# Performance work log

Hardware: AMD Instinct MI355X
Metric: run time of the kernel (lower is better)

The kernel has to match this reference:

```python
import jax, jax.numpy as jnp
import numpy as np

B, CIN, H, W = 4, 1024, 64, 64
PLANES = 256
K = 3
DIL = 2
PAD = DIL * (K - 1) // 2  # = 2
EPS = 1e-5


def setup_inputs() -> dict:
    key = jax.random.key(0)
    ks = jax.random.split(key, 16)
    d = {}
    d['x'] = jax.random.normal(ks[0], (B, CIN, H, W), dtype=jnp.float32)
    # conv1: 1x1, inplanes->planes, no bias
    d['w1'] = jax.random.normal(ks[1], (PLANES, CIN), dtype=jnp.float32) * 0.02
    d['gamma1'] = jnp.ones((PLANES,), jnp.float32)
    d['beta1'] = jnp.zeros((PLANES,), jnp.float32)
    d['mean1'] = jax.random.normal(ks[2], (PLANES,), dtype=jnp.float32) * 0.1
    d['var1'] = jax.random.uniform(ks[3], (PLANES,), minval=0.5, maxval=1.5, dtype=jnp.float32)
    # deform_offset: 3x3 conv planes->18, with bias
    d['woff'] = jax.random.normal(ks[4], (18, PLANES, K, K), dtype=jnp.float32) * 0.01
    d['boff'] = jnp.zeros((18,), jnp.float32)
    # conv2 (deformable): 3x3 planes->planes, with bias
    d['w2'] = jax.random.normal(ks[5], (PLANES, PLANES, K, K), dtype=jnp.float32) * 0.02
    d['bconv2'] = jnp.zeros((PLANES,), jnp.float32)
    d['gamma2'] = jnp.ones((PLANES,), jnp.float32)
    d['beta2'] = jnp.zeros((PLANES,), jnp.float32)
    d['mean2'] = jax.random.normal(ks[6], (PLANES,), dtype=jnp.float32) * 0.1
    d['var2'] = jax.random.uniform(ks[7], (PLANES,), minval=0.5, maxval=1.5, dtype=jnp.float32)
    # conv3: 1x1 planes->planes*4, no bias
    d['w3'] = jax.random.normal(ks[8], (PLANES * 4, PLANES), dtype=jnp.float32) * 0.02
    d['gamma3'] = jnp.ones((PLANES * 4,), jnp.float32)
    d['beta3'] = jnp.zeros((PLANES * 4,), jnp.float32)
    d['mean3'] = jax.random.normal(ks[9], (PLANES * 4,), dtype=jnp.float32) * 0.1
    d['var3'] = jax.random.uniform(ks[10], (PLANES * 4,), minval=0.5, maxval=1.5, dtype=jnp.float32)
    return d


def _bn(x, gamma, beta, mean, var):
    # inference-mode BatchNorm over channel dim (NCHW)
    inv = jax.lax.rsqrt(var + EPS)
    return (x - mean[:, None, None]) * (inv * gamma)[:, None, None] + beta[:, None, None]


def _deform_conv(x, offset, w, b):
    # x: [B,C,H,W]; offset: [B,18,H,W] ordered (dy,dx) per kernel tap; w: [O,C,3,3]
    Bn, C, Hh, Ww = x.shape
    off = offset.reshape(Bn, K * K, 2, Hh, Ww)
    off_y, off_x = off[:, :, 0], off[:, :, 1]          # [B,9,H,W]
    kk = jnp.arange(K * K)
    base_y = (kk // K) * DIL - PAD                      # [9]
    base_x = (kk % K) * DIL - PAD
    ys = jnp.arange(Hh, dtype=x.dtype)
    xs = jnp.arange(Ww, dtype=x.dtype)
    py = base_y.astype(x.dtype)[None, :, None, None] + ys[None, None, :, None] + off_y
    px = base_x.astype(x.dtype)[None, :, None, None] + xs[None, None, None, :] + off_x

    def sample_one(img, py1, px1):
        # img [C,H,W]; py1/px1 [9,H,W] -> [C,9,H,W] bilinear with zero padding
        y0 = jnp.floor(py1)
        x0 = jnp.floor(px1)
        wy = py1 - y0
        wx = px1 - x0

        def gather(yc, xc):
            yi = yc.astype(jnp.int32)
            xi = xc.astype(jnp.int32)
            valid = ((yi >= 0) & (yi < Hh) & (xi >= 0) & (xi < Ww)).astype(img.dtype)
            yi = jnp.clip(yi, 0, Hh - 1)
            xi = jnp.clip(xi, 0, Ww - 1)
            return img[:, yi, xi] * valid[None]

        v00 = gather(y0, x0)
        v01 = gather(y0, x0 + 1)
        v10 = gather(y0 + 1, x0)
        v11 = gather(y0 + 1, x0 + 1)
        return (v00 * ((1 - wy) * (1 - wx))[None] + v01 * ((1 - wy) * wx)[None]
                + v10 * (wy * (1 - wx))[None] + v11 * (wy * wx)[None])

    sampled = jax.vmap(sample_one)(x, py, px)           # [B,C,9,H,W]
    out = jnp.einsum('bckhw,ock->bohw', sampled, w.reshape(w.shape[0], C, K * K))
    return out + b[None, :, None, None]


def reference(x, w1, gamma1, beta1, mean1, var1, woff, boff, w2, bconv2,
              gamma2, beta2, mean2, var2, w3, gamma3, beta3, mean3, var3):
    residual = x
    out = jnp.einsum('bchw,oc->bohw', x, w1)            # conv1 1x1
    out = jax.nn.relu(_bn(out, gamma1, beta1, mean1, var1))
    offset = jax.lax.conv_general_dilated(
        out, woff, window_strides=(1, 1), padding=((PAD, PAD), (PAD, PAD)),
        rhs_dilation=(DIL, DIL), dimension_numbers=('NCHW', 'OIHW', 'NCHW'))
    offset = offset + boff[None, :, None, None]
    out = _deform_conv(out, offset, w2, bconv2)
    out = jax.nn.relu(_bn(out, gamma2, beta2, mean2, var2))
    out = jnp.einsum('bchw,oc->bohw', out, w3)          # conv3 1x1
    out = _bn(out, gamma3, beta3, mean3, var3)
    return jax.nn.relu(out + residual)
```

## Files before the change

### kernel.cpp

```cpp
#include <hip/hip_runtime.h>

#define EPS_BN 1e-5f

typedef __bf16 bf16x8 __attribute__((ext_vector_type(8)));
typedef float f32x4 __attribute__((ext_vector_type(4)));

__device__ __forceinline__ unsigned short f2bf(float f) {
  union { float f; unsigned u; } v; v.f = f;
  unsigned r = v.u + 0x7fffu + ((v.u >> 16) & 1u);
  return (unsigned short)(r >> 16);
}
__device__ __forceinline__ float bf2f(unsigned short h) {
  union { unsigned u; float f; } v; v.u = ((unsigned)h) << 16;
  return v.f;
}

__global__ __launch_bounds__(256) void prep_all(
    const float* __restrict__ w1, const float* __restrict__ w2, const float* __restrict__ woff,
    const float* __restrict__ w3,
    const float* g1, const float* b1, const float* m1, const float* v1,
    const float* g2, const float* b2, const float* m2, const float* v2, const float* bconv2,
    const float* g3, const float* b3, const float* m3, const float* v3,
    unsigned short* __restrict__ w1b, unsigned short* __restrict__ w2r,
    uint4* __restrict__ act1Pz, unsigned short* __restrict__ wob,
    unsigned short* __restrict__ w3b, float* __restrict__ shift3,
    float* s1, float* h1, float* s2, float* h2) {
  int bid = blockIdx.x, tid = threadIdx.x;
  if (bid < 1024) {
    int i = bid * 256 + tid;
    w1b[i] = f2bf(w1[i]);
  } else if (bid < 3328) {
    int i = (bid - 1024) * 256 + tid;
    int o = i / 2304, r = i % 2304;
    int kk = r / 256, c = r % 256;
    w2r[i] = f2bf(w2[(size_t)o * 2304 + c * 9 + kk]);
  } else if (bid < 5640) {
    int i = (bid - 3328) * 256 + tid;
    if (i < 591872) act1Pz[i] = uint4{0, 0, 0, 0};
  } else if (bid < 5928) {
    int i = (bid - 5640) * 256 + tid;
    int o = i / 2304, r = i % 2304;
    int kk = r / 256, c = r % 256;
    wob[i] = (o < 18) ? f2bf(woff[(size_t)o * 2304 + c * 9 + kk]) : (unsigned short)0;
  } else if (bid < 6952) {
    int i = (bid - 5928) * 256 + tid;
    int o = i >> 8;
    float sc = rsqrtf(v3[o] + EPS_BN) * g3[o];
    w3b[i] = f2bf(w3[i] * sc);
  } else if (bid < 6956) {
    int c = (bid - 6952) * 256 + tid;
    float sc = rsqrtf(v3[c] + EPS_BN) * g3[c];
    shift3[c] = b3[c] - m3[c] * sc;
  } else {
    int c = tid;
    float sc1 = rsqrtf(v1[c] + EPS_BN) * g1[c];
    s1[c] = sc1; h1[c] = b1[c] - m1[c] * sc1;
    float sc2 = rsqrtf(v2[c] + EPS_BN) * g2[c];
    s2[c] = sc2; h2[c] = b2[c] + (bconv2[c] - m2[c]) * sc2;
  }
}

__global__ __launch_bounds__(256) void transpose_x(const float* __restrict__ x,
                                                   unsigned short* __restrict__ xT) {
  __shared__ float t[32][33];
  int b = blockIdx.z;
  int p0 = blockIdx.x * 32, c0 = blockIdx.y * 32;
  int tx = threadIdx.x & 31, ty = threadIdx.x >> 5;
  const float* xb = x + (size_t)b * 1024 * 4096;
#pragma unroll
  for (int j = 0; j < 4; ++j) {
    int c = c0 + ty + j * 8;
    t[ty + j * 8][tx] = xb[(size_t)c * 4096 + p0 + tx];
  }
  __syncthreads();
  unsigned short* xTb = xT + (size_t)b * 4096 * 1024;
  int pl = threadIdx.x >> 3;
  int cl = (threadIdx.x & 7) * 4;
  float v0 = t[cl][pl], v1 = t[cl + 1][pl], v2 = t[cl + 2][pl], v3 = t[cl + 3][pl];
  uint2 pk;
  pk.x = (unsigned)f2bf(v0) | ((unsigned)f2bf(v1) << 16);
  pk.y = (unsigned)f2bf(v2) | ((unsigned)f2bf(v3) << 16);
  *(uint2*)(xTb + (size_t)(p0 + pl) * 1024 + c0 + cl) = pk;
}

__global__ __launch_bounds__(256) void gemm_split(
    const unsigned short* __restrict__ A, const unsigned short* __restrict__ Bm,
    unsigned short* __restrict__ part, int M, int N, int K, int KH) {
  __shared__ __align__(16) char smem[32768];
  unsigned short* sA0 = (unsigned short*)smem;
  unsigned short* sB0 = (unsigned short*)(smem + 8192);
  unsigned short* sA1 = (unsigned short*)(smem + 16384);
  unsigned short* sB1 = (unsigned short*)(smem + 24576);
  float* tbuf = (float*)smem;
  int tid = threadIdx.x, lane = tid & 63, wv = tid >> 6;
  int z = blockIdx.z;
  int m0 = blockIdx.y * 128, n0 = blockIdx.x * 128;
  f32x4 acc[4][4] = {};
  int rowA = tid >> 2;
  int kcol = (tid & 3) * 8;
  int wm = wv & 1, wn = wv >> 1;
  int lane15 = lane & 15, quad8 = (lane >> 4) * 8, quad = lane >> 4;

#define GS_STAGE(dA, dB, K0)                                                              \
  {                                                                                       \
    int k0_ = (K0);                                                                       \
    _Pragma("unroll") for (int r = 0; r < 2; ++r) {                                       \
      const unsigned short* gp = A + (size_t)(m0 + r * 64 + rowA) * K + k0_ + kcol;       \
      __builtin_amdgcn_global_load_lds((const __attribute__((address_space(1))) void*)gp, \
          (__attribute__((address_space(3))) void*)&(dA)[r * 2048 + wv * 512], 16, 0, 0); \
    }                                                                                     \
    _Pragma("unroll") for (int r = 0; r < 2; ++r) {                                       \
      const unsigned short* gp = Bm + (size_t)(n0 + r * 64 + rowA) * K + k0_ + kcol;      \
      __builtin_amdgcn_global_load_lds((const __attribute__((address_space(1))) void*)gp, \
          (__attribute__((address_space(3))) void*)&(dB)[r * 2048 + wv * 512], 16, 0, 0); \
    }                                                                                     \
  }

#define GS_COMPUTE(dA, dB)                                                                \
  {                                                                                       \
    bf16x8 afr[4], bfr[4];                                                                \
    _Pragma("unroll") for (int mi = 0; mi < 4; ++mi)                                      \
      afr[mi] = *(const bf16x8*)&(dA)[(wm * 64 + mi * 16 + lane15) * 32 + quad8];         \
    _Pragma("unroll") for (int ni = 0; ni < 4; ++ni)                                      \
      bfr[ni] = *(const bf16x8*)&(dB)[(wn * 64 + ni * 16 + lane15) * 32 + quad8];         \
    _Pragma("unroll") for (int mi = 0; mi < 4; ++mi)                                      \
      _Pragma("unroll") for (int ni = 0; ni < 4; ++ni)                                    \
        acc[mi][ni] =                                                                     \
            __builtin_amdgcn_mfma_f32_16x16x32_bf16(afr[mi], bfr[ni], acc[mi][ni], 0, 0, 0); \
  }

  int kbase = z * KH;
  int nst = KH >> 5;
  GS_STAGE(sA0, sB0, kbase);
  __syncthreads();
  for (int t = 0; t < nst; t += 2) {
    GS_STAGE(sA1, sB1, kbase + (t + 1) * 32);
    GS_COMPUTE(sA0, sB0);
    __syncthreads();
    if (t + 2 < nst) GS_STAGE(sA0, sB0, kbase + (t + 2) * 32);
    GS_COMPUTE(sA1, sB1);
    __syncthreads();
  }
#undef GS_STAGE
#undef GS_COMPUTE

  unsigned short* outH = part + (size_t)z * M * N;
  int trow = tid >> 3;
  int tcol16 = (tid & 7) * 16;
  int growBase = m0 + (trow >> 4) * 64 + (trow & 15);
#pragma unroll
  for (int mi = 0; mi < 4; ++mi) {
    __syncthreads();
#pragma unroll
    for (int ni = 0; ni < 4; ++ni)
#pragma unroll
      for (int reg = 0; reg < 4; ++reg)
        tbuf[(wm * 16 + quad * 4 + reg) * 132 + wn * 64 + ni * 16 + lane15] = acc[mi][ni][reg];
    __syncthreads();
    int gr = growBase + mi * 16;
    const float* lp = &tbuf[trow * 132 + tcol16];
    unsigned o[8];
#pragma unroll
    for (int j = 0; j < 8; ++j)
      o[j] = (unsigned)f2bf(lp[2 * j]) | ((unsigned)f2bf(lp[2 * j + 1]) << 16);
    unsigned short* op = outH + (size_t)gr * 256 + n0 + tcol16;
    *(uint4*)(op) = uint4{o[0], o[1], o[2], o[3]};
    *(uint4*)(op + 8) = uint4{o[4], o[5], o[6], o[7]};
  }
}

template <int NS, int PAD>
__global__ __launch_bounds__(256) void epi_bn(const unsigned short* __restrict__ part,
                                              const float* __restrict__ scale,
                                              const float* __restrict__ shift,
                                              unsigned short* __restrict__ outT,
                                              unsigned short* __restrict__ outP) {
  int gid = blockIdx.x * 256 + threadIdx.x;
  int row = gid >> 5, c0 = (gid & 31) * 8;
  float v[8] = {};
#pragma unroll
  for (int s = 0; s < NS; ++s) {
    uint4 q = *(const uint4*)(part + (size_t)s * 16384 * 256 + (size_t)row * 256 + c0);
    unsigned u[4] = {q.x, q.y, q.z, q.w};
#pragma unroll
    for (int j = 0; j < 4; ++j) {
      v[2 * j]     += bf2f((unsigned short)(u[j] & 0xffffu));
      v[2 * j + 1] += bf2f((unsigned short)(u[j] >> 16));
    }
  }
  float sc[8], sh[8];
  *(float4*)&sc[0] = *(const float4*)(scale + c0); *(float4*)&sc[4] = *(const float4*)(scale + c0 + 4);
  *(float4*)&sh[0] = *(const float4*)(shift + c0); *(float4*)&sh[4] = *(const float4*)(shift + c0 + 4);
  unsigned o[4];
#pragma unroll
  for (int j = 0; j < 4; ++j) {
    float lo = fmaxf(v[2 * j] * sc[2 * j] + sh[2 * j], 0.f);
    float hi = fmaxf(v[2 * j + 1] * sc[2 * j + 1] + sh[2 * j + 1], 0.f);
    o[j] = (unsigned)f2bf(lo) | ((unsigned)f2bf(hi) << 16);
  }
  uint4 pk{o[0], o[1], o[2], o[3]};
  *(uint4*)(outT + (size_t)row * 256 + c0) = pk;
  if constexpr (PAD) {
    int bb = row >> 12, p = row & 4095;
    *(uint4*)(outP + (((size_t)(bb * 68) + (p >> 6) + 2) * 68 + (p & 63) + 2) * 256 + c0) = pk;
  }
}

__global__ __launch_bounds__(256) void gemm_res(
    const unsigned short* __restrict__ A, const unsigned short* __restrict__ Bm,
    float* __restrict__ outp, const float* __restrict__ shift3,
    const float* __restrict__ resid, int M, int N, int K, long bStrideB, long bStrideOut) {
  __shared__ __align__(16) char smem[32768];
  unsigned short* sA0 = (unsigned short*)smem;
  unsigned short* sB0 = (unsigned short*)(smem + 8192);
  unsigned short* sA1 = (unsigned short*)(smem + 16384);
  unsigned short* sB1 = (unsigned short*)(smem + 24576);
  float* tbuf = (float*)smem;
  int tid = threadIdx.x, lane = tid & 63, wv = tid >> 6;
  int z = blockIdx.z;
  const unsigned short* Bz = Bm + (size_t)z * bStrideB;
  int m0 = blockIdx.y * 128, n0 = blockIdx.x * 128;
  f32x4 acc[4][4] = {};
  int rowA = tid >> 2;
  int kcol = (tid & 3) * 8;
  int wm = wv & 1, wn = wv >> 1;
  int lane15 = lane & 15, quad8 = (lane >> 4) * 8, quad = lane >> 4;

#define GR_STAGE(dA, dB, K0)                                                              \
  {                                                                                       \
    int k0_ = (K0);                                                                       \
    _Pragma("unroll") for (int r = 0; r < 2; ++r) {                                       \
      const unsigned short* gp = A + (size_t)(m0 + r * 64 + rowA) * K + k0_ + kcol;       \
      __builtin_amdgcn_global_load_lds((const __attribute__((address_space(1))) void*)gp, \
          (__attribute__((address_space(3))) void*)&(dA)[r * 2048 + wv * 512], 16, 0, 0); \
    }                                                                                     \
    _Pragma("unroll") for (int r = 0; r < 2; ++r) {                                       \
      const unsigned short* gp = Bz + (size_t)(n0 + r * 64 + rowA) * K + k0_ + kcol;      \
      __builtin_amdgcn_global_load_lds((const __attribute__((address_space(1))) void*)gp, \
          (__attribute__((address_space(3))) void*)&(dB)[r * 2048 + wv * 512], 16, 0, 0); \
    }                                                                                     \
  }

#define GR_COMPUTE(dA, dB)                                                                \
  {                                                                                       \
    bf16x8 afr[4], bfr[4];                                                                \
    _Pragma("unroll") for (int mi = 0; mi < 4; ++mi)                                      \
      afr[mi] = *(const bf16x8*)&(dA)[(wm * 64 + mi * 16 + lane15) * 32 + quad8];         \
    _Pragma("unroll") for (int ni = 0; ni < 4; ++ni)                                      \
      bfr[ni] = *(const bf16x8*)&(dB)[(wn * 64 + ni * 16 + lane15) * 32 + quad8];         \
    _Pragma("unroll") for (int mi = 0; mi < 4; ++mi)                                      \
      _Pragma("unroll") for (int ni = 0; ni < 4; ++ni)                                    \
        acc[mi][ni] =                                                                     \
            __builtin_amdgcn_mfma_f32_16x16x32_bf16(afr[mi], bfr[ni], acc[mi][ni], 0, 0, 0); \
  }

  int nst = K >> 5;
  GR_STAGE(sA0, sB0, 0);
  __syncthreads();
  for (int t = 0; t < nst; t += 2) {
    GR_STAGE(sA1, sB1, (t + 1) * 32);
    GR_COMPUTE(sA0, sB0);
    __syncthreads();
    if (t + 2 < nst) GR_STAGE(sA0, sB0, (t + 2) * 32);
    GR_COMPUTE(sA1, sB1);
    __syncthreads();
  }
#undef GR_STAGE
#undef GR_COMPUTE

  float* outF = outp + (size_t)z * bStrideOut;
  const float* res = resid + (size_t)z * bStrideOut;
  int trow = tid >> 3;
  int tcol = (tid & 7) * 4;
  int growBase = m0 + (trow >> 4) * 64 + (trow & 15);
#pragma unroll
  for (int mi = 0; mi < 4; ++mi) {
    __syncthreads();
#pragma unroll
    for (int ni = 0; ni < 4; ++ni)
#pragma unroll
      for (int reg = 0; reg < 4; ++reg)
        tbuf[(wm * 16 + quad * 4 + reg) * 132 + wn * 64 + ni * 16 + lane15] = acc[mi][ni][reg];
    __syncthreads();
    int gr = growBase + mi * 16;
    float sh = shift3[gr];
    const float* rp = res + (size_t)gr * N + n0 + tcol;
    float* op = outF + (size_t)gr * N + n0 + tcol;
    const float* lp = &tbuf[trow * 132 + tcol];
#pragma unroll
    for (int j = 0; j < 4; ++j) {
      float4 rv = *(const float4*)(rp + j * 32);
      float4 lv = *(const float4*)(lp + j * 32);
      float4 ov;
      ov.x = fmaxf(lv.x + sh + rv.x, 0.f);
      ov.y = fmaxf(lv.y + sh + rv.y, 0.f);
      ov.z = fmaxf(lv.z + sh + rv.z, 0.f);
      ov.w = fmaxf(lv.w + sh + rv.w, 0.f);
      *(float4*)(op + j * 32) = ov;
    }
  }
}

__global__ __launch_bounds__(256) void off_gemm(const unsigned short* __restrict__ actP,
                                                const unsigned short* __restrict__ wob,
                                                const float* __restrict__ boff,
                                                float* __restrict__ offsP) {
  __shared__ __align__(16) char smem[24576];
  unsigned short* sA0 = (unsigned short*)smem;
  unsigned short* sB0 = (unsigned short*)(smem + 8192);
  unsigned short* sA1 = (unsigned short*)(smem + 12288);
  unsigned short* sB1 = (unsigned short*)(smem + 20480);
  int tid = threadIdx.x, lane = tid & 63, wv = tid >> 6;
  int m0 = blockIdx.x * 64;
  int lane15 = lane & 15, quad8 = (lane >> 4) * 8;
  int rowA = tid >> 3;
  int kc = (tid & 7) * 8;

  const unsigned short* baseA[2];
#pragma unroll
  for (int r = 0; r < 2; ++r) {
    int row = m0 + r * 32 + rowA;
    int b = row >> 12, p = row & 4095;
    baseA[r] = actP + (((size_t)(b * 68) + (p >> 6) + 2) * 68 + (p & 63) + 2) * 256 + kc;
  }
  const unsigned short* baseB = wob + (size_t)rowA * 2304 + kc;

  f32x4 acc[2] = {};

#define OG_STAGE(dA, dB, S)                                                               \
  {                                                                                       \
    int s_ = (S); int kk_ = s_ >> 2; int c0_ = (s_ & 3) * 64;                             \
    long shift_ = (long)(((kk_ / 3) * 2 - 2) * 68 + ((kk_ % 3) * 2 - 2));                 \
    _Pragma("unroll") for (int r = 0; r < 2; ++r) {                                       \
      const unsigned short* gp = baseA[r] + shift_ * 256 + c0_;                           \
      __builtin_amdgcn_global_load_lds((const __attribute__((address_space(1))) void*)gp, \
          (__attribute__((address_space(3))) void*)&(dA)[r * 2048 + wv * 512], 16, 0, 0); \
    }                                                                                     \
    {                                                                                     \
      const unsigned short* gp = baseB + kk_ * 256 + c0_;                                 \
      __builtin_amdgcn_global_load_lds((const __attribute__((address_space(1))) void*)gp, \
          (__attribute__((address_space(3))) void*)&(dB)[wv * 512], 16, 0, 0);            \
    }                                                                                     \
  }

#define OG_COMPUTE(dA, dB)                                                                \
  {                                                                                       \
    bf16x8 afr[2], bfr[2][2];                                                             \
    _Pragma("unroll") for (int kq = 0; kq < 2; ++kq) {                                    \
      afr[kq] = *(const bf16x8*)&(dA)[(wv * 16 + lane15) * 64 + kq * 32 + quad8];         \
      _Pragma("unroll") for (int ni = 0; ni < 2; ++ni)                                    \
        bfr[kq][ni] = *(const bf16x8*)&(dB)[(ni * 16 + lane15) * 64 + kq * 32 + quad8];   \
    }                                                                                     \
    _Pragma("unroll") for (int kq = 0; kq < 2; ++kq)                                      \
      _Pragma("unroll") for (int ni = 0; ni < 2; ++ni)                                    \
        acc[ni] = __builtin_amdgcn_mfma_f32_16x16x32_bf16(afr[kq], bfr[kq][ni], acc[ni], 0, 0, 0); \
  }

  OG_STAGE(sA0, sB0, 0);
  __syncthreads();
  for (int s = 0; s < 36; s += 2) {
    OG_STAGE(sA1, sB1, s + 1);
    OG_COMPUTE(sA0, sB0);
    __syncthreads();
    if (s + 2 < 36) OG_STAGE(sA0, sB0, s + 2);
    OG_COMPUTE(sA1, sB1);
    __syncthreads();
  }
#undef OG_STAGE
#undef OG_COMPUTE

#pragma unroll
  for (int ni = 0; ni < 2; ++ni) {
    int o = ni * 16 + lane15;
    if (o < 18) {
      float bo = boff[o];
#pragma unroll
      for (int reg = 0; reg < 4; ++reg) {
        int row = m0 + wv * 16 + (lane >> 4) * 4 + reg;
        offsP[(size_t)row * 18 + o] = acc[ni][reg] + bo;
      }
    }
  }
}

__global__ __launch_bounds__(256) void deform_sample(const unsigned short* __restrict__ act1T,
                                                     const float* __restrict__ offsP,
                                                     unsigned short* __restrict__ S) {
  int g = threadIdx.x >> 5, t = threadIdx.x & 31;
  int idx = blockIdx.x * 8 + g;
  int b = idx >> 12, p = idx & 4095;
  int h = p >> 6, w = p & 63;
  const unsigned short* actb = act1T + (size_t)b * 4096 * 256 + t * 8;
  unsigned short* Sp = S + (size_t)idx * 2304 + t * 8;
  float ov = (t < 18) ? offsP[(size_t)idx * 18 + t] : 0.f;
#pragma unroll
  for (int kk = 0; kk < 9; ++kk) {
    float offy = __shfl(ov, 2 * kk, 32);
    float offx = __shfl(ov, 2 * kk + 1, 32);
    float py = (float)(h + (kk / 3) * 2 - 2) + offy;
    float px = (float)(w + (kk % 3) * 2 - 2) + offx;
    float fy = floorf(py), fx = floorf(px);
    int y0 = (int)fy, x0 = (int)fx;
    float wy = py - fy, wx = px - fx;
    bool yv0 = (y0 >= 0 && y0 < 64), yv1 = (y0 >= -1 && y0 < 63);
    bool xv0 = (x0 >= 0 && x0 < 64), xv1 = (x0 >= -1 && x0 < 63);
    const unsigned short* cb = actb + (y0 * 64 + x0) * 256;
    uint4 q00{0,0,0,0}, q01{0,0,0,0}, q10{0,0,0,0}, q11{0,0,0,0};
    if (yv0 && xv0) q00 = *(const uint4*)(cb);
    if (yv0 && xv1) q01 = *(const uint4*)(cb + 256);
    if (yv1 && xv0) q10 = *(const uint4*)(cb + 64 * 256);
    if (yv1 && xv1) q11 = *(const uint4*)(cb + 64 * 256 + 256);
    float w00 = (1.f - wy) * (1.f - wx), w01 = (1.f - wy) * wx;
    float w10 = wy * (1.f - wx), w11 = wy * wx;
    unsigned u00[4] = {q00.x, q00.y, q00.z, q00.w};
    unsigned u01[4] = {q01.x, q01.y, q01.z, q01.w};
    unsigned u10[4] = {q10.x, q10.y, q10.z, q10.w};
    unsigned u11[4] = {q11.x, q11.y, q11.z, q11.w};
    unsigned out[4];
#pragma unroll
    for (int j = 0; j < 4; ++j) {
      float lo = bf2f((unsigned short)(u00[j] & 0xffffu)) * w00 +
                 bf2f((unsigned short)(u01[j] & 0xffffu)) * w01 +
                 bf2f((unsigned short)(u10[j] & 0xffffu)) * w10 +
                 bf2f((unsigned short)(u11[j] & 0xffffu)) * w11;
      float hi = bf2f((unsigned short)(u00[j] >> 16)) * w00 +
                 bf2f((unsigned short)(u01[j] >> 16)) * w01 +
                 bf2f((unsigned short)(u10[j] >> 16)) * w10 +
                 bf2f((unsigned short)(u11[j] >> 16)) * w11;
      out[j] = (unsigned)f2bf(lo) | ((unsigned)f2bf(hi) << 16);
    }
    *(uint4*)(Sp + kk * 256) = uint4{out[0], out[1], out[2], out[3]};
  }
}

extern "C" void kernel_launch(void* const* d_in, const int* in_sizes, int n_in,
                              void* d_out, int out_size, void* d_ws, size_t ws_size,
                              hipStream_t stream) {
  const float* x      = (const float*)d_in[0];
  const float* w1     = (const float*)d_in[1];
  const float* gamma1 = (const float*)d_in[2];
  const float* beta1  = (const float*)d_in[3];
  const float* mean1  = (const float*)d_in[4];
  const float* var1   = (const float*)d_in[5];
  const float* woff   = (const float*)d_in[6];
  const float* boff   = (const float*)d_in[7];
  const float* w2     = (const float*)d_in[8];
  const float* bconv2 = (const float*)d_in[9];
  const float* gamma2 = (const float*)d_in[10];
  const float* beta2  = (const float*)d_in[11];
  const float* mean2  = (const float*)d_in[12];
  const float* var2   = (const float*)d_in[13];
  const float* w3     = (const float*)d_in[14];
  const float* gamma3 = (const float*)d_in[15];
  const float* beta3  = (const float*)d_in[16];
  const float* mean3  = (const float*)d_in[17];
  const float* var3   = (const float*)d_in[18];

  char* ws = (char*)d_ws;
  unsigned short* xT    = (unsigned short*)(ws);
  unsigned short* act1T = (unsigned short*)(ws + 33554432);
  unsigned short* act2T = (unsigned short*)(ws + 41943040);
  unsigned short* S     = (unsigned short*)(ws + 50331648);
  float*          offs  = (float*)(ws + 125829120);
  unsigned short* w1b   = (unsigned short*)(ws + 127008768);
  unsigned short* w2r   = (unsigned short*)(ws + 127533056);
  unsigned short* w3b   = (unsigned short*)(ws + 128712704);
  float*          bnS1  = (float*)(ws + 129236992);
  float*          bnH1  = (float*)(ws + 129238016);
  float*          bnS2  = (float*)(ws + 129239040);
  float*          bnH2  = (float*)(ws + 129240064);
  float*          shift3= (float*)(ws + 129241088);
  unsigned short* act1P = S;
  unsigned short* part1 = (unsigned short*)(ws + 62914560);
  unsigned short* part2 = (unsigned short*)ws;
  unsigned short* wob   = act2T;

  prep_all<<<6957, 256, 0, stream>>>(w1, w2, woff, w3,
                                     gamma1, beta1, mean1, var1,
                                     gamma2, beta2, mean2, var2, bconv2,
                                     gamma3, beta3, mean3, var3,
                                     w1b, w2r, (uint4*)act1P, wob, w3b, shift3,
                                     bnS1, bnH1, bnS2, bnH2);
  transpose_x<<<dim3(128, 32, 4), 256, 0, stream>>>(x, xT);

  gemm_split<<<dim3(2, 128, 4), 256, 0, stream>>>(xT, w1b, part1, 16384, 256, 1024, 256);
  epi_bn<4, 1><<<2048, 256, 0, stream>>>(part1, bnS1, bnH1, act1T, act1P);

  off_gemm<<<256, 256, 0, stream>>>(act1P, wob, boff, offs);
  deform_sample<<<dim3(2048), 256, 0, stream>>>(act1T, offs, S);

  gemm_split<<<dim3(2, 128, 4), 256, 0, stream>>>(S, w2r, part2, 16384, 256, 2304, 576);
  epi_bn<4, 0><<<2048, 256, 0, stream>>>(part2, bnS2, bnH2, act2T, nullptr);

  gemm_res<<<dim3(32, 8, 4), 256, 0, stream>>>(w3b, act2T, (float*)d_out, shift3, x,
                                               1024, 4096, 256, 4096L * 256, 4194304L);
}
```

Baseline: 307.5 us.

## Replace syncthreads with vmcnt-targeted waits and halve split-K factor

In the three GEMM kernels, the full __syncthreads after each staged async global-to-LDS load is replaced by explicit s_waitcnt vmcnt(N) plus a raw s_barrier. Each wait only drains the previous stage's loads, so the next stage's loads stay in flight while compute runs. Shared buffers are split into separate arrays to keep them distinct. The split-K factor for the two main GEMMs also drops from 4 to 2, which halves partial-sum traffic in the epilogue but leaves fewer blocks for parallelism. The hand-counted vmcnt values risk race conditions if the compiler emits a different number of memory ops than assumed.

```diff
diff --git a/kernel.cpp b/kernel.cpp
--- a/kernel.cpp
+++ b/kernel.cpp
@@ -86,12 +86,12 @@
 __global__ __launch_bounds__(256) void gemm_split(
     const unsigned short* __restrict__ A, const unsigned short* __restrict__ Bm,
     unsigned short* __restrict__ part, int M, int N, int K, int KH) {
-  __shared__ __align__(16) char smem[32768];
-  unsigned short* sA0 = (unsigned short*)smem;
-  unsigned short* sB0 = (unsigned short*)(smem + 8192);
-  unsigned short* sA1 = (unsigned short*)(smem + 16384);
-  unsigned short* sB1 = (unsigned short*)(smem + 24576);
-  float* tbuf = (float*)smem;
+  __shared__ __align__(16) char blob[16896];
+  __shared__ __align__(16) unsigned short sA1[4096];
+  __shared__ __align__(16) unsigned short sB1[4096];
+  unsigned short* sA0 = (unsigned short*)blob;
+  unsigned short* sB0 = (unsigned short*)(blob + 8192);
+  float* tbuf = (float*)blob;
   int tid = threadIdx.x, lane = tid & 63, wv = tid >> 6;
   int z = blockIdx.z;
   int m0 = blockIdx.y * 128, n0 = blockIdx.x * 128;
@@ -132,14 +132,21 @@
   int kbase = z * KH;
   int nst = KH >> 5;
   GS_STAGE(sA0, sB0, kbase);
-  __syncthreads();
   for (int t = 0; t < nst; t += 2) {
     GS_STAGE(sA1, sB1, kbase + (t + 1) * 32);
+    asm volatile("s_waitcnt vmcnt(4)" ::: "memory");
+    __builtin_amdgcn_s_barrier();
     GS_COMPUTE(sA0, sB0);
-    __syncthreads();
-    if (t + 2 < nst) GS_STAGE(sA0, sB0, kbase + (t + 2) * 32);
+    __builtin_amdgcn_s_barrier();
+    if (t + 2 < nst) {
+      GS_STAGE(sA0, sB0, kbase + (t + 2) * 32);
+      asm volatile("s_waitcnt vmcnt(4)" ::: "memory");
+    } else {
+      asm volatile("s_waitcnt vmcnt(0)" ::: "memory");
+    }
+    __builtin_amdgcn_s_barrier();
     GS_COMPUTE(sA1, sB1);
-    __syncthreads();
+    __builtin_amdgcn_s_barrier();
   }
 #undef GS_STAGE
 #undef GS_COMPUTE
@@ -210,12 +217,12 @@
     const unsigned short* __restrict__ A, const unsigned short* __restrict__ Bm,
     float* __restrict__ outp, const float* __restrict__ shift3,
     const float* __restrict__ resid, int M, int N, int K, long bStrideB, long bStrideOut) {
-  __shared__ __align__(16) char smem[32768];
-  unsigned short* sA0 = (unsigned short*)smem;
-  unsigned short* sB0 = (unsigned short*)(smem + 8192);
-  unsigned short* sA1 = (unsigned short*)(smem + 16384);
-  unsigned short* sB1 = (unsigned short*)(smem + 24576);
-  float* tbuf = (float*)smem;
+  __shared__ __align__(16) char blob[16896];
+  __shared__ __align__(16) unsigned short sA1[4096];
+  __shared__ __align__(16) unsigned short sB1[4096];
+  unsigned short* sA0 = (unsigned short*)blob;
+  unsigned short* sB0 = (unsigned short*)(blob + 8192);
+  float* tbuf = (float*)blob;
   int tid = threadIdx.x, lane = tid & 63, wv = tid >> 6;
   int z = blockIdx.z;
   const unsigned short* Bz = Bm + (size_t)z * bStrideB;
@@ -256,14 +263,21 @@
 
   int nst = K >> 5;
   GR_STAGE(sA0, sB0, 0);
-  __syncthreads();
   for (int t = 0; t < nst; t += 2) {
     GR_STAGE(sA1, sB1, (t + 1) * 32);
+    asm volatile("s_waitcnt vmcnt(4)" ::: "memory");
+    __builtin_amdgcn_s_barrier();
     GR_COMPUTE(sA0, sB0);
-    __syncthreads();
-    if (t + 2 < nst) GR_STAGE(sA0, sB0, (t + 2) * 32);
+    __builtin_amdgcn_s_barrier();
+    if (t + 2 < nst) {
+      GR_STAGE(sA0, sB0, (t + 2) * 32);
+      asm volatile("s_waitcnt vmcnt(4)" ::: "memory");
+    } else {
+      asm volatile("s_waitcnt vmcnt(0)" ::: "memory");
+    }
+    __builtin_amdgcn_s_barrier();
     GR_COMPUTE(sA1, sB1);
-    __syncthreads();
+    __builtin_amdgcn_s_barrier();
   }
 #undef GR_STAGE
 #undef GR_COMPUTE
@@ -305,11 +319,10 @@
                                                 const unsigned short* __restrict__ wob,
                                                 const float* __restrict__ boff,
                                                 float* __restrict__ offsP) {
-  __shared__ __align__(16) char smem[24576];
-  unsigned short* sA0 = (unsigned short*)smem;
-  unsigned short* sB0 = (unsigned short*)(smem + 8192);
-  unsigned short* sA1 = (unsigned short*)(smem + 12288);
-  unsigned short* sB1 = (unsigned short*)(smem + 20480);
+  __shared__ __align__(16) unsigned short sA0[4096];
+  __shared__ __align__(16) unsigned short sB0[2048];
+  __shared__ __align__(16) unsigned short sA1[4096];
+  __shared__ __align__(16) unsigned short sB1[2048];
   int tid = threadIdx.x, lane = tid & 63, wv = tid >> 6;
   int m0 = blockIdx.x * 64;
   int lane15 = lane & 15, quad8 = (lane >> 4) * 8;
@@ -357,14 +370,21 @@
   }
 
   OG_STAGE(sA0, sB0, 0);
-  __syncthreads();
   for (int s = 0; s < 36; s += 2) {
     OG_STAGE(sA1, sB1, s + 1);
+    asm volatile("s_waitcnt vmcnt(3)" ::: "memory");
+    __builtin_amdgcn_s_barrier();
     OG_COMPUTE(sA0, sB0);
-    __syncthreads();
-    if (s + 2 < 36) OG_STAGE(sA0, sB0, s + 2);
+    __builtin_amdgcn_s_barrier();
+    if (s + 2 < 36) {
+      OG_STAGE(sA0, sB0, s + 2);
+      asm volatile("s_waitcnt vmcnt(3)" ::: "memory");
+    } else {
+      asm volatile("s_waitcnt vmcnt(0)" ::: "memory");
+    }
+    __builtin_amdgcn_s_barrier();
     OG_COMPUTE(sA1, sB1);
-    __syncthreads();
+    __builtin_amdgcn_s_barrier();
   }
 #undef OG_STAGE
 #undef OG_COMPUTE
@@ -483,14 +503,14 @@
                                      bnS1, bnH1, bnS2, bnH2);
   transpose_x<<<dim3(128, 32, 4), 256, 0, stream>>>(x, xT);
 
-  gemm_split<<<dim3(2, 128, 4), 256, 0, stream>>>(xT, w1b, part1, 16384, 256, 1024, 256);
-  epi_bn<4, 1><<<2048, 256, 0, stream>>>(part1, bnS1, bnH1, act1T, act1P);
+  gemm_split<<<dim3(2, 128, 2), 256, 0, stream>>>(xT, w1b, part1, 16384, 256, 1024, 512);
+  epi_bn<2, 1><<<2048, 256, 0, stream>>>(part1, bnS1, bnH1, act1T, act1P);
 
   off_gemm<<<256, 256, 0, stream>>>(act1P, wob, boff, offs);
   deform_sample<<<dim3(2048), 256, 0, stream>>>(act1T, offs, S);
 
-  gemm_split<<<dim3(2, 128, 4), 256, 0, stream>>>(S, w2r, part2, 16384, 256, 2304, 576);
-  epi_bn<4, 0><<<2048, 256, 0, stream>>>(part2, bnS2, bnH2, act2T, nullptr);
+  gemm_split<<<dim3(2, 128, 2), 256, 0, stream>>>(S, w2r, part2, 16384, 256, 2304, 1152);
+  epi_bn<2, 0><<<2048, 256, 0, stream>>>(part2, bnS2, bnH2, act2T, nullptr);
 
   gemm_res<<<dim3(32, 8, 4), 256, 0, stream>>>(w3b, act2T, (float*)d_out, shift3, x,
                                                1024, 4096, 256, 4096L * 256, 4194304L);
```

New measurement: 285.1 us. 1.08x faster.
